# Kernel optimization log

Hardware: AMD Instinct MI355X
Metric: run time of the kernel (lower is better)

Reference implementation:

```python
import jax, jax.numpy as jnp
import numpy as np

N_RULES = 64  # R
OUT_PER_RULE = 64  # O, fc out = R*O = 4096


def setup_inputs() -> dict:
    key = jax.random.key(0)
    k1, k2, k3, k4 = jax.random.split(key, 4)
    S, D_IN = 8192, 1024
    RO = N_RULES * OUT_PER_RULE
    X = jax.random.normal(k1, (S, D_IN), dtype=jnp.float32)
    # torch.nn.Linear-style weight [out, in] and bias [out]
    W = jax.random.normal(k2, (RO, D_IN), dtype=jnp.float32) * (1.0 / np.sqrt(D_IN))
    b = jax.random.normal(k3, (RO,), dtype=jnp.float32) * 0.01
    # rule firing strengths (computed under no_grad in the original)
    lambdas = jax.random.uniform(k4, (S, N_RULES), dtype=jnp.float32)
    return {"X": X, "W": W, "b": b, "lambdas": lambdas}


def reference(X, W, b, lambdas):
    # fc + sigmoid: [S, R*O]
    H = jax.nn.sigmoid(X @ W.T + b)
    S = H.shape[0]
    # apply_rule_strength: block-diagonal lambda_eye @ H^T is exactly a
    # rule-weighted sum over the R consecutive O-sized blocks of H.
    Hr = H.reshape(S, N_RULES, OUT_PER_RULE)  # [S, R, O]
    Y = jnp.einsum("sr,sro->so", lambdas, Hr)  # [S, O]
    return Y
```

## Files before the change

### kernel.cpp

```cpp
#include <hip/hip_runtime.h>

#define S_DIM 8192
#define K_DIM 1024
#define RO_DIM 4096
#define O_DIM 64
#define SO (S_DIM * O_DIM)
#define NSLICE 16

typedef __attribute__((ext_vector_type(8))) __bf16 bf16x8;
typedef __attribute__((ext_vector_type(4))) float floatx4;
typedef __attribute__((ext_vector_type(4))) unsigned short ushx4;
typedef __attribute__((ext_vector_type(8))) unsigned short ushx8;

__device__ inline unsigned short f2bf(float f) {
  unsigned u = __builtin_bit_cast(unsigned, f);
  u += 0x7fff + ((u >> 16) & 1);
  return (unsigned short)(u >> 16);
}
__device__ inline float bf2f(unsigned short h) {
  unsigned u = ((unsigned)h) << 16;
  return __builtin_bit_cast(float, u);
}

__global__ __launch_bounds__(256) void cast_kernel(const float* __restrict__ X,
                                                   const float* __restrict__ W,
                                                   unsigned short* __restrict__ Xb,
                                                   unsigned short* __restrict__ Wb) {
  const int NX4 = (S_DIM * K_DIM) / 4;
#pragma unroll
  for (int i = 0; i < 4; ++i) {
    int g = blockIdx.x * 1024 + i * 256 + threadIdx.x;
    float4 v;
    unsigned short* dst;
    if (g < NX4) {
      v = ((const float4*)X)[g];
      dst = Xb + (size_t)g * 4;
    } else {
      int j = g - NX4;
      v = ((const float4*)W)[j];
      dst = Wb + (size_t)j * 4;
    }
    ushx4 o;
    o.x = f2bf(v.x); o.y = f2bf(v.y); o.z = f2bf(v.z); o.w = f2bf(v.w);
    *(ushx4*)dst = o;
  }
}


template <int MB>
__device__ __forceinline__ void rdA(bf16x8 (&af)[2][2], const unsigned short* As,
                                    int cA0, int cA1) {
  af[0][0] = *(const bf16x8*)(As + MB * 1024 + cA0);
  af[0][1] = *(const bf16x8*)(As + MB * 1024 + cA1);
  af[1][0] = *(const bf16x8*)(As + (MB + 1) * 1024 + cA0);
  af[1][1] = *(const bf16x8*)(As + (MB + 1) * 1024 + cA1);
}

template <int MB>
__device__ __forceinline__ void mfma8(floatx4 (&acc)[8][4], const bf16x8 (&af)[2][2],
                                      const bf16x8 (&bfr)[4][2]) {
  __builtin_amdgcn_s_setprio(1);
#pragma unroll
  for (int ii = 0; ii < 2; ++ii)
#pragma unroll
    for (int ni = 0; ni < 4; ++ni) {
      acc[MB + ii][ni] = __builtin_amdgcn_mfma_f32_16x16x32_bf16(
          af[ii][0], bfr[ni][0], acc[MB + ii][ni], 0, 0, 0);
      acc[MB + ii][ni] = __builtin_amdgcn_mfma_f32_16x16x32_bf16(
          af[ii][1], bfr[ni][1], acc[MB + ii][ni], 0, 0, 0);
    }
  __builtin_amdgcn_s_setprio(0);
}

#define BAR() __builtin_amdgcn_s_barrier()
#define LGKM0() asm volatile("s_waitcnt lgkmcnt(0)" ::: "memory")

__global__ __launch_bounds__(512, 2) void gemm_kernel(const unsigned short* __restrict__ Xb,
                                                      const unsigned short* __restrict__ Wb,
                                                      const float* __restrict__ bias,
                                                      const float* __restrict__ lam,
                                                      unsigned short* __restrict__ partial) {
  __shared__ __align__(16) unsigned char smem[135168];
  unsigned short* sm = (unsigned short*)smem;
  float* lamsh = (float*)(smem + 131072);

  const int t = threadIdx.x;
  const int lane = t & 63;
  const int w = t >> 6;
  const int wm = w >> 2;
  const int wn = w & 3;
  const int quad = lane >> 4;
  const int l16 = lane & 15;

  int id = blockIdx.y * 16 + blockIdx.x;
  int swz = (id & 7) * 64 + (id >> 3);
  const int bx = swz & 15;
  const int by = swz >> 4;
  const int gm0 = by * 256;
  const int gn0 = bx * 256;

  const int rowt = t >> 3;
  const int gcc = (t & 7) ^ (rowt & 7);
  const size_t goff = (size_t)rowt * K_DIM + (size_t)gcc * 8;
  const unsigned short* Abase = Xb + (size_t)gm0 * K_DIM;
  const unsigned short* Bbase = Wb + (size_t)gn0 * K_DIM;

  auto STAGE = [&](const unsigned short* gbase, int half, int ktile, int slotOff) {
#pragma unroll
    for (int j = 0; j < 2; ++j) {
      const unsigned short* src =
          gbase + (size_t)(half * 128 + j * 64) * K_DIM + ktile * 64 + goff;
      __builtin_amdgcn_global_load_lds(
          (const __attribute__((address_space(1))) void*)src,
          (__attribute__((address_space(3))) void*)(sm + slotOff + j * 4096 + t * 8),
          16, 0, 0);
    }
  };

  STAGE(Abase, 0, 0, 0);
  STAGE(Abase, 1, 0, 8192);
  STAGE(Bbase, 0, 0, 16384);
  STAGE(Bbase, 1, 0, 24576);
  STAGE(Bbase, 0, 1, 32768 + 16384);
  STAGE(Bbase, 1, 1, 32768 + 24576);

  {
    int i = t;
    lamsh[i] = lam[(size_t)(gm0 + (i >> 2)) * 64 + bx * 4 + (i & 3)];
    i = t + 512;
    lamsh[i] = lam[(size_t)(gm0 + (i >> 2)) * 64 + bx * 4 + (i & 3)];
  }
  asm volatile("s_waitcnt vmcnt(4)" ::: "memory");
  BAR();

  floatx4 acc[8][4];
#pragma unroll
  for (int ni = 0; ni < 4; ++ni) {
    float bv = bias[gn0 + wn * 64 + ni * 16 + l16];
#pragma unroll
    for (int mi = 0; mi < 8; ++mi) acc[mi][ni] = (floatx4){bv, bv, bv, bv};
  }

  const int cA0 = ((quad) ^ (l16 & 7)) * 8;
  const int cA1 = ((4 + quad) ^ (l16 & 7)) * 8;

  for (int kt = 0; kt < 16; ++kt) {
    const int b = kt & 1;
    const unsigned short* As = sm + b * 32768 + wm * 8192 + l16 * 64;
    const unsigned short* Bs =
        sm + b * 32768 + 16384 + (wn >> 1) * 8192 + ((wn & 1) * 64 + l16) * 64;
    const int bufA = ((kt + 1) & 1) * 32768;
    const int bufB = b * 32768;

    bf16x8 bfr[4][2], af[2][2];

#pragma unroll
    for (int ni = 0; ni < 4; ++ni) {
      bfr[ni][0] = *(const bf16x8*)(Bs + ni * 1024 + cA0);
      bfr[ni][1] = *(const bf16x8*)(Bs + ni * 1024 + cA1);
    }
    rdA<0>(af, As, cA0, cA1);
    if (kt < 15) STAGE(Abase, 0, kt + 1, bufA + 0);
    BAR();
    LGKM0();
    mfma8<0>(acc, af, bfr);
    BAR();

    rdA<2>(af, As, cA0, cA1);
    if (kt < 15) STAGE(Abase, 1, kt + 1, bufA + 8192);
    BAR();
    LGKM0();
    mfma8<2>(acc, af, bfr);
    BAR();

    rdA<4>(af, As, cA0, cA1);
    if (kt < 14) STAGE(Bbase, 0, kt + 2, bufB + 16384);
    BAR();
    LGKM0();
    mfma8<4>(acc, af, bfr);
    BAR();

    rdA<6>(af, As, cA0, cA1);
    if (kt < 14) {
      STAGE(Bbase, 1, kt + 2, bufB + 24576);
      asm volatile("s_waitcnt vmcnt(4)" ::: "memory");
    } else if (kt == 14) {
      asm volatile("s_waitcnt vmcnt(0)" ::: "memory");
    }
    BAR();
    LGKM0();
    mfma8<6>(acc, af, bfr);
    BAR();
  }

  __syncthreads();
  {
    unsigned short* yreg = sm + wn * 16384;
#pragma unroll
    for (int mi = 0; mi < 8; ++mi) {
#pragma unroll
      for (int r = 0; r < 4; ++r) {
        int row = wm * 128 + mi * 16 + quad * 4 + r;
        float lamv = lamsh[row * 4 + wn];
#pragma unroll
        for (int ni = 0; ni < 4; ++ni) {
          float sg = 1.f / (1.f + __expf(-acc[mi][ni][r]));
          yreg[row * 64 + ((ni ^ quad) * 16) + l16] = f2bf(lamv * sg);
        }
      }
    }
  }
  __syncthreads();
  {
    unsigned short* pb = partial + (size_t)bx * SO + (size_t)gm0 * 64;
#pragma unroll
    for (int g = 0; g < 4; ++g) {
      int idx = g * 4096 + t * 8;
      int row = idx >> 6;
      int c = idx & 63;
      int phys = row * 64 + ((((c >> 4) ^ ((row >> 2) & 3))) << 4) + (c & 15);
      float s[8];
#pragma unroll
      for (int j = 0; j < 8; ++j) s[j] = 0.f;
#pragma unroll
      for (int q = 0; q < 4; ++q) {
        ushx8 v = *(const ushx8*)(sm + q * 16384 + phys);
#pragma unroll
        for (int j = 0; j < 8; ++j) s[j] += bf2f(v[j]);
      }
      ushx8 o;
#pragma unroll
      for (int j = 0; j < 8; ++j) o[j] = f2bf(s[j]);
      *(ushx8*)(pb + idx) = o;
    }
  }
}

__global__ __launch_bounds__(256) void reduce_kernel(const unsigned short* __restrict__ partial,
                                                     float* __restrict__ Y) {
  int i4 = blockIdx.x * 256 + threadIdx.x;
  float s0 = 0.f, s1 = 0.f, s2 = 0.f, s3 = 0.f;
#pragma unroll
  for (int c = 0; c < NSLICE; ++c) {
    ushx4 v = ((const ushx4*)(partial + (size_t)c * SO))[i4];
    s0 += bf2f(v.x); s1 += bf2f(v.y); s2 += bf2f(v.z); s3 += bf2f(v.w);
  }
  ((float4*)Y)[i4] = (float4){s0, s1, s2, s3};
}

extern "C" void kernel_launch(void* const* d_in, const int* in_sizes, int n_in,
                              void* d_out, int out_size, void* d_ws, size_t ws_size,
                              hipStream_t stream) {
  const float* X = (const float*)d_in[0];
  const float* W = (const float*)d_in[1];
  const float* b = (const float*)d_in[2];
  const float* lam = (const float*)d_in[3];
  float* Y = (float*)d_out;

  unsigned short* Xb = (unsigned short*)d_ws;
  unsigned short* Wb = Xb + (size_t)S_DIM * K_DIM;
  unsigned short* partial = Wb + (size_t)RO_DIM * K_DIM;

  int nCast = ((S_DIM + RO_DIM) * K_DIM / 4) / 1024;
  cast_kernel<<<nCast, 256, 0, stream>>>(X, W, Xb, Wb);

  dim3 g(RO_DIM / 256, S_DIM / 256);
  gemm_kernel<<<g, 512, 0, stream>>>(Xb, Wb, b, lam, partial);

  reduce_kernel<<<SO / 1024, 256, 0, stream>>>(partial, Y);
}
```

Before: 167.7 us.

## Replace partial buffer and reduce kernel with atomic adds, restructure MFMA k-loop

The cross-column-tile reduction now uses float atomic adds straight into Y, which the cast kernel zeroes first. This removes the bf16 partial buffer, its writes and reads, and the separate reduce kernel launch. The k-loop changes from 2x4 MFMA sub-steps to 4x2 quadrants with register reuse of A and B fragments, and adds sched_barriers. The B layout in LDS and the block swizzle (adjacent column tiles grouped) are also changed. The risks are atomic contention on Y from 16 column tiles per row block and a final sum order that is not deterministic.

```diff
diff --git a/kernel.cpp b/kernel.cpp
--- a/kernel.cpp
+++ b/kernel.cpp
@@ -5,7 +5,6 @@
 #define RO_DIM 4096
 #define O_DIM 64
 #define SO (S_DIM * O_DIM)
-#define NSLICE 16
 
 typedef __attribute__((ext_vector_type(8))) __bf16 bf16x8;
 typedef __attribute__((ext_vector_type(4))) float floatx4;
@@ -25,8 +24,11 @@
 __global__ __launch_bounds__(256) void cast_kernel(const float* __restrict__ X,
                                                    const float* __restrict__ W,
                                                    unsigned short* __restrict__ Xb,
-                                                   unsigned short* __restrict__ Wb) {
+                                                   unsigned short* __restrict__ Wb,
+                                                   float* __restrict__ Y) {
   const int NX4 = (S_DIM * K_DIM) / 4;
+  int zi = blockIdx.x * 256 + threadIdx.x;
+  if (zi < SO / 4) ((float4*)Y)[zi] = (float4){0.f, 0.f, 0.f, 0.f};
 #pragma unroll
   for (int i = 0; i < 4; ++i) {
     int g = blockIdx.x * 1024 + i * 256 + threadIdx.x;
@@ -47,39 +49,31 @@
 }
 
 
-template <int MB>
-__device__ __forceinline__ void rdA(bf16x8 (&af)[2][2], const unsigned short* As,
-                                    int cA0, int cA1) {
-  af[0][0] = *(const bf16x8*)(As + MB * 1024 + cA0);
-  af[0][1] = *(const bf16x8*)(As + MB * 1024 + cA1);
-  af[1][0] = *(const bf16x8*)(As + (MB + 1) * 1024 + cA0);
-  af[1][1] = *(const bf16x8*)(As + (MB + 1) * 1024 + cA1);
-}
-
-template <int MB>
-__device__ __forceinline__ void mfma8(floatx4 (&acc)[8][4], const bf16x8 (&af)[2][2],
+template <int MB, int NB>
+__device__ __forceinline__ void mfmaq(floatx4 (&acc)[8][4], const bf16x8 (&afr)[4][2],
                                       const bf16x8 (&bfr)[4][2]) {
   __builtin_amdgcn_s_setprio(1);
 #pragma unroll
-  for (int ii = 0; ii < 2; ++ii)
-#pragma unroll
-    for (int ni = 0; ni < 4; ++ni) {
-      acc[MB + ii][ni] = __builtin_amdgcn_mfma_f32_16x16x32_bf16(
-          af[ii][0], bfr[ni][0], acc[MB + ii][ni], 0, 0, 0);
-      acc[MB + ii][ni] = __builtin_amdgcn_mfma_f32_16x16x32_bf16(
-          af[ii][1], bfr[ni][1], acc[MB + ii][ni], 0, 0, 0);
+  for (int m = 0; m < 4; ++m)
+#pragma unroll
+    for (int n = 0; n < 2; ++n) {
+      acc[MB + m][NB + n] = __builtin_amdgcn_mfma_f32_16x16x32_bf16(
+          afr[m][0], bfr[NB + n][0], acc[MB + m][NB + n], 0, 0, 0);
+      acc[MB + m][NB + n] = __builtin_amdgcn_mfma_f32_16x16x32_bf16(
+          afr[m][1], bfr[NB + n][1], acc[MB + m][NB + n], 0, 0, 0);
     }
   __builtin_amdgcn_s_setprio(0);
 }
 
 #define BAR() __builtin_amdgcn_s_barrier()
 #define LGKM0() asm volatile("s_waitcnt lgkmcnt(0)" ::: "memory")
+#define SB0() __builtin_amdgcn_sched_barrier(0)
 
 __global__ __launch_bounds__(512, 2) void gemm_kernel(const unsigned short* __restrict__ Xb,
                                                       const unsigned short* __restrict__ Wb,
                                                       const float* __restrict__ bias,
                                                       const float* __restrict__ lam,
-                                                      unsigned short* __restrict__ partial) {
+                                                      float* __restrict__ Y) {
   __shared__ __align__(16) unsigned char smem[135168];
   unsigned short* sm = (unsigned short*)smem;
   float* lamsh = (float*)(smem + 131072);
@@ -93,9 +87,10 @@
   const int l16 = lane & 15;
 
   int id = blockIdx.y * 16 + blockIdx.x;
-  int swz = (id & 7) * 64 + (id >> 3);
-  const int bx = swz & 15;
-  const int by = swz >> 4;
+  int x = id & 7;
+  int j = id >> 3;
+  const int bx = 2 * x + (j & 1);
+  const int by = j >> 1;
   const int gm0 = by * 256;
   const int gn0 = bx * 256;
 
@@ -107,12 +102,12 @@
 
   auto STAGE = [&](const unsigned short* gbase, int half, int ktile, int slotOff) {
 #pragma unroll
-    for (int j = 0; j < 2; ++j) {
+    for (int jj = 0; jj < 2; ++jj) {
       const unsigned short* src =
-          gbase + (size_t)(half * 128 + j * 64) * K_DIM + ktile * 64 + goff;
+          gbase + (size_t)(half * 128 + jj * 64) * K_DIM + ktile * 64 + goff;
       __builtin_amdgcn_global_load_lds(
           (const __attribute__((address_space(1))) void*)src,
-          (__attribute__((address_space(3))) void*)(sm + slotOff + j * 4096 + t * 8),
+          (__attribute__((address_space(3))) void*)(sm + slotOff + jj * 4096 + t * 8),
           16, 0, 0);
     }
   };
@@ -147,40 +142,53 @@
   for (int kt = 0; kt < 16; ++kt) {
     const int b = kt & 1;
     const unsigned short* As = sm + b * 32768 + wm * 8192 + l16 * 64;
-    const unsigned short* Bs =
-        sm + b * 32768 + 16384 + (wn >> 1) * 8192 + ((wn & 1) * 64 + l16) * 64;
-    const int bufA = ((kt + 1) & 1) * 32768;
+    const unsigned short* Bs = sm + b * 32768 + 16384 + wn * 4096 + l16 * 64;
+    const int bufA = (b ^ 1) * 32768;
     const int bufB = b * 32768;
 
-    bf16x8 bfr[4][2], af[2][2];
-
-#pragma unroll
-    for (int ni = 0; ni < 4; ++ni) {
-      bfr[ni][0] = *(const bf16x8*)(Bs + ni * 1024 + cA0);
-      bfr[ni][1] = *(const bf16x8*)(Bs + ni * 1024 + cA1);
-    }
-    rdA<0>(af, As, cA0, cA1);
-    if (kt < 15) STAGE(Abase, 0, kt + 1, bufA + 0);
+    bf16x8 afr[4][2], bfr[4][2];
+
+#pragma unroll
+    for (int m = 0; m < 4; ++m) {
+      afr[m][0] = *(const bf16x8*)(As + m * 1024 + cA0);
+      afr[m][1] = *(const bf16x8*)(As + m * 1024 + cA1);
+    }
+#pragma unroll
+    for (int n = 0; n < 2; ++n) {
+      bfr[n][0] = *(const bf16x8*)(Bs + n * 1024 + cA0);
+      bfr[n][1] = *(const bf16x8*)(Bs + n * 1024 + cA1);
+    }
+    if (kt < 15) STAGE(Abase, 0, kt + 1, bufA);
     BAR();
     LGKM0();
-    mfma8<0>(acc, af, bfr);
-    BAR();
-
-    rdA<2>(af, As, cA0, cA1);
+    SB0();
+    mfmaq<0, 0>(acc, afr, bfr);
+    BAR();
+
+#pragma unroll
+    for (int n = 2; n < 4; ++n) {
+      bfr[n][0] = *(const bf16x8*)(Bs + n * 1024 + cA0);
+      bfr[n][1] = *(const bf16x8*)(Bs + n * 1024 + cA1);
+    }
     if (kt < 15) STAGE(Abase, 1, kt + 1, bufA + 8192);
     BAR();
     LGKM0();
-    mfma8<2>(acc, af, bfr);
-    BAR();
-
-    rdA<4>(af, As, cA0, cA1);
+    SB0();
+    mfmaq<0, 2>(acc, afr, bfr);
+    BAR();
+
+#pragma unroll
+    for (int m = 0; m < 4; ++m) {
+      afr[m][0] = *(const bf16x8*)(As + (4 + m) * 1024 + cA0);
+      afr[m][1] = *(const bf16x8*)(As + (4 + m) * 1024 + cA1);
+    }
     if (kt < 14) STAGE(Bbase, 0, kt + 2, bufB + 16384);
     BAR();
     LGKM0();
-    mfma8<4>(acc, af, bfr);
-    BAR();
-
-    rdA<6>(af, As, cA0, cA1);
+    SB0();
+    mfmaq<4, 0>(acc, afr, bfr);
+    BAR();
+
     if (kt < 14) {
       STAGE(Bbase, 1, kt + 2, bufB + 24576);
       asm volatile("s_waitcnt vmcnt(4)" ::: "memory");
@@ -188,8 +196,8 @@
       asm volatile("s_waitcnt vmcnt(0)" ::: "memory");
     }
     BAR();
-    LGKM0();
-    mfma8<6>(acc, af, bfr);
+    SB0();
+    mfmaq<4, 2>(acc, afr, bfr);
     BAR();
   }
 
@@ -212,7 +220,7 @@
   }
   __syncthreads();
   {
-    unsigned short* pb = partial + (size_t)bx * SO + (size_t)gm0 * 64;
+    float* Yb = Y + (size_t)gm0 * 64;
 #pragma unroll
     for (int g = 0; g < 4; ++g) {
       int idx = g * 4096 + t * 8;
@@ -221,31 +229,17 @@
       int phys = row * 64 + ((((c >> 4) ^ ((row >> 2) & 3))) << 4) + (c & 15);
       float s[8];
 #pragma unroll
-      for (int j = 0; j < 8; ++j) s[j] = 0.f;
+      for (int jj = 0; jj < 8; ++jj) s[jj] = 0.f;
 #pragma unroll
       for (int q = 0; q < 4; ++q) {
         ushx8 v = *(const ushx8*)(sm + q * 16384 + phys);
 #pragma unroll
-        for (int j = 0; j < 8; ++j) s[j] += bf2f(v[j]);
+        for (int jj = 0; jj < 8; ++jj) s[jj] += bf2f(v[jj]);
       }
-      ushx8 o;
-#pragma unroll
-      for (int j = 0; j < 8; ++j) o[j] = f2bf(s[j]);
-      *(ushx8*)(pb + idx) = o;
-    }
-  }
-}
-
-__global__ __launch_bounds__(256) void reduce_kernel(const unsigned short* __restrict__ partial,
-                                                     float* __restrict__ Y) {
-  int i4 = blockIdx.x * 256 + threadIdx.x;
-  float s0 = 0.f, s1 = 0.f, s2 = 0.f, s3 = 0.f;
-#pragma unroll
-  for (int c = 0; c < NSLICE; ++c) {
-    ushx4 v = ((const ushx4*)(partial + (size_t)c * SO))[i4];
-    s0 += bf2f(v.x); s1 += bf2f(v.y); s2 += bf2f(v.z); s3 += bf2f(v.w);
-  }
-  ((float4*)Y)[i4] = (float4){s0, s1, s2, s3};
+#pragma unroll
+      for (int jj = 0; jj < 8; ++jj) unsafeAtomicAdd(Yb + idx + jj, s[jj]);
+    }
+  }
 }
 
 extern "C" void kernel_launch(void* const* d_in, const int* in_sizes, int n_in,
@@ -259,13 +253,10 @@
 
   unsigned short* Xb = (unsigned short*)d_ws;
   unsigned short* Wb = Xb + (size_t)S_DIM * K_DIM;
-  unsigned short* partial = Wb + (size_t)RO_DIM * K_DIM;
 
   int nCast = ((S_DIM + RO_DIM) * K_DIM / 4) / 1024;
-  cast_kernel<<<nCast, 256, 0, stream>>>(X, W, Xb, Wb);
+  cast_kernel<<<nCast, 256, 0, stream>>>(X, W, Xb, Wb, Y);
 
   dim3 g(RO_DIM / 256, S_DIM / 256);
-  gemm_kernel<<<g, 512, 0, stream>>>(Xb, Wb, b, lam, partial);
-
-  reduce_kernel<<<SO / 1024, 256, 0, stream>>>(partial, Y);
-}
+  gemm_kernel<<<g, 512, 0, stream>>>(Xb, Wb, b, lam, Y);
+}
```

Result: slower. 465.3 us (+177.4%).
